# Kernel optimization log

Measured on AMD Instinct MI355X. Metric: run time of the kernel, lower is better.

The kernel has to match this reference:

```python
import jax, jax.numpy as jnp
import numpy as np

B, S, D, H, KH, DH, L, V, MULT = 1, 2048, 2048, 16, 2, 128, 4, 10000, 4
INNER = D * MULT
EPS = 1e-5


def layernorm(x, g, b):
    m = jnp.mean(x, axis=-1, keepdims=True)
    v = jnp.var(x, axis=-1, keepdims=True)
    return (x - m) * jax.lax.rsqrt(v + EPS) * g + b


def setup_inputs() -> dict:
    key = jax.random.key(0)
    ks = jax.random.split(key, 24)
    s = lambda *shape: 0.02
    inp = {
        'text': jax.random.randint(ks[0], (B, S), 0, V),
        'embed_w': jax.random.normal(ks[1], (V, D), jnp.float32) * 0.02,
        # model-level LayerNorm (applied after embed and after every block)
        'model_norm_g': jnp.ones((D,), jnp.float32),
        'model_norm_b': jnp.zeros((D,), jnp.float32),
        # per-block params, stacked on leading L axis
        'blk_norm_g': jnp.ones((L, D), jnp.float32),
        'blk_norm_b': jnp.zeros((L, D), jnp.float32),
        'attn_norm_g': jnp.ones((L, D), jnp.float32),  # RingAttention prenorm
        'attn_norm_b': jnp.zeros((L, D), jnp.float32),
        'wq': jax.random.normal(ks[2], (L, D, H * DH), jnp.float32) * 0.02,
        'wk': jax.random.normal(ks[3], (L, D, KH * DH), jnp.float32) * 0.02,
        'wv': jax.random.normal(ks[4], (L, D, KH * DH), jnp.float32) * 0.02,
        'wo': jax.random.normal(ks[5], (L, H * DH, D), jnp.float32) * 0.02,
        'qn_g': jnp.ones((L, DH), jnp.float32),  # qk_norm LayerNorm scales
        'kn_g': jnp.ones((L, DH), jnp.float32),
        'w1': jax.random.normal(ks[6], (L, D, INNER), jnp.float32) * 0.02,
        'b1': jnp.zeros((L, INNER), jnp.float32),
        'w2': jax.random.normal(ks[7], (L, INNER, D), jnp.float32) * 0.02,
        'b2': jnp.zeros((L, D), jnp.float32),
        # output head: LayerNorm + Linear(D, V)
        'head_norm_g': jnp.ones((D,), jnp.float32),
        'head_norm_b': jnp.zeros((D,), jnp.float32),
        'head_w': jax.random.normal(ks[8], (D, V), jnp.float32) * 0.02,
        'head_b': jnp.zeros((V,), jnp.float32),
    }
    return inp


def _attention(xn, wq, wk, wv, wo, qn_g, kn_g):
    # xn: [B,S,D] (already prenormed)
    q = (xn @ wq).reshape(B, S, H, DH)
    k = (xn @ wk).reshape(B, S, KH, DH)
    v = (xn @ wv).reshape(B, S, KH, DH)
    # qk-norm: LayerNorm over head dim with learnable scale
    q = layernorm(q, qn_g, 0.0)
    k = layernorm(k, kn_g, 0.0)
    # GQA: expand kv heads to query heads
    rep = H // KH
    k = jnp.repeat(k, rep, axis=2)  # [B,S,H,DH]
    v = jnp.repeat(v, rep, axis=2)
    scale = DH ** -0.5
    scores = jnp.einsum('bqhd,bkhd->bhqk', q, k) * scale  # [B,H,S,S]
    causal = jnp.tril(jnp.ones((S, S), bool))
    scores = jnp.where(causal, scores, jnp.finfo(scores.dtype).min)
    p = jax.nn.softmax(scores, axis=-1)
    out = jnp.einsum('bhqk,bkhd->bqhd', p, v).reshape(B, S, H * DH)
    return out @ wo


def reference(text, embed_w, model_norm_g, model_norm_b, blk_norm_g, blk_norm_b,
              attn_norm_g, attn_norm_b, wq, wk, wv, wo, qn_g, kn_g,
              w1, b1, w2, b2, head_norm_g, head_norm_b, head_w, head_b):
    x = embed_w[text]                                # [B,S,D]
    x = layernorm(x, model_norm_g, model_norm_b)
    for i in range(L):
        h = layernorm(x, blk_norm_g[i], blk_norm_b[i])       # block norm
        hn = layernorm(h, attn_norm_g[i], attn_norm_b[i])    # attn prenorm
        h = _attention(hn, wq[i], wk[i], wv[i], wo[i], qn_g[i], kn_g[i]) + h
        ff = jax.nn.gelu(h @ w1[i] + b1[i]) @ w2[i] + b2[i]
        x = ff + h
        x = layernorm(x, model_norm_g, model_norm_b)
    x = layernorm(x, head_norm_g, head_norm_b)
    return x @ head_w + head_b                       # [B,S,V] logits
```

## Files before the change

kernel.cpp:

```cpp
#include <hip/hip_runtime.h>
#include <math.h>

#define S_LEN 2048
#define DMODEL 2048
#define NHEAD 16
#define KVHEAD 2
#define DHEAD 128
#define NLAYER 4
#define VOCAB 10000
#define INNER_DIM 8192
#define LN_EPS 1e-5f
#define VOCAB_PAD 10240
#define QKVN 2560

typedef __attribute__((ext_vector_type(4))) float f32x4;
typedef __attribute__((ext_vector_type(2))) float f32x2;
typedef __attribute__((ext_vector_type(8))) short s16x8;
typedef __attribute__((ext_vector_type(4))) short s16x4;

__device__ __forceinline__ short f2bf(float f) {
  union { float f; unsigned u; } v; v.f = f;
  unsigned r = v.u + 0x7FFFu + ((v.u >> 16) & 1u);
  return (short)(r >> 16);
}

__device__ __forceinline__ float gelu_tanh(float x) {
  float z = 0.7978845608028654f * (x + 0.044715f * x * x * x);
  float t = __expf(-2.0f * fabsf(z));
  float th = (1.0f - t) / (1.0f + t);
  th = copysignf(th, z);
  return 0.5f * x * (1.0f + th);
}

__device__ __forceinline__ void glds16(const void* g, void* l) {
  __builtin_amdgcn_global_load_lds(
      (const __attribute__((address_space(1))) unsigned int*)g,
      (__attribute__((address_space(3))) unsigned int*)l, 16, 0, 0);
}

__global__ __launch_bounds__(256)
void wtrans_all(const float* __restrict__ wq, const float* __restrict__ wk,
                const float* __restrict__ wv, const float* __restrict__ wo,
                const float* __restrict__ w1, const float* __restrict__ w2,
                short* __restrict__ wqkvT, short* __restrict__ woT,
                short* __restrict__ w1T, short* __restrict__ w2T) {
  __shared__ float ld[64][65];
  int b = blockIdx.x;
  const float* W; short* WT; int gx, K;
  if (b < 1024)      { W = wq; WT = wqkvT; gx = 32; K = 2048; }
  else if (b < 1152) { b -= 1024; W = wk; WT = wqkvT + (size_t)2048 * 2048; gx = 4; K = 2048; }
  else if (b < 1280) { b -= 1152; W = wv; WT = wqkvT + (size_t)2304 * 2048; gx = 4; K = 2048; }
  else if (b < 2304) { b -= 1280; W = wo; WT = woT; gx = 32; K = 2048; }
  else if (b < 6400) { b -= 2304; W = w1; WT = w1T; gx = 128; K = 2048; }
  else               { b -= 6400; W = w2; WT = w2T; gx = 32; K = 8192; }
  const int N = gx * 64;
  const int n0 = (b % gx) * 64, k0 = (b / gx) * 64;
  const int tid = threadIdx.x;
  const int rbase = tid >> 4;
  const int c4 = (tid & 15) * 4;
#pragma unroll
  for (int q = 0; q < 4; ++q) {
    int kk = rbase + q * 16;
    f32x4 v = *(const f32x4*)(W + (size_t)(k0 + kk) * N + n0 + c4);
    ld[kk][c4 + 0] = v[0]; ld[kk][c4 + 1] = v[1];
    ld[kk][c4 + 2] = v[2]; ld[kk][c4 + 3] = v[3];
  }
  __syncthreads();
#pragma unroll
  for (int s = 0; s < 2; ++s) {
    int lin = tid + s * 256;
    int nn = lin >> 3;
    int ks = lin & 7;
    s16x8 o;
#pragma unroll
    for (int j = 0; j < 8; ++j) o[j] = f2bf(ld[ks * 8 + j][nn]);
    *(s16x8*)&WT[(size_t)(n0 + nn) * K + k0 + ks * 8] = o;
  }
}

__global__ __launch_bounds__(256)
void wtrans64(const float* __restrict__ W, short* __restrict__ WT,
              int K, int N, int NP) {
  __shared__ float ld[64][65];
  const int n0 = blockIdx.x * 64, k0 = blockIdx.y * 64;
  const int tid = threadIdx.x;
  const int rbase = tid >> 4;
  const int c4 = (tid & 15) * 4;
#pragma unroll
  for (int q = 0; q < 4; ++q) {
    int kk = rbase + q * 16;
    const float* wp = W + (size_t)(k0 + kk) * N + n0 + c4;
    float v0, v1, v2, v3;
    if (n0 + c4 + 3 < N) {
      f32x4 v = *(const f32x4*)wp;
      v0 = v[0]; v1 = v[1]; v2 = v[2]; v3 = v[3];
    } else {
      v0 = (n0 + c4 + 0 < N) ? wp[0] : 0.f;
      v1 = (n0 + c4 + 1 < N) ? wp[1] : 0.f;
      v2 = (n0 + c4 + 2 < N) ? wp[2] : 0.f;
      v3 = (n0 + c4 + 3 < N) ? wp[3] : 0.f;
    }
    ld[kk][c4 + 0] = v0; ld[kk][c4 + 1] = v1;
    ld[kk][c4 + 2] = v2; ld[kk][c4 + 3] = v3;
  }
  __syncthreads();
#pragma unroll
  for (int s = 0; s < 2; ++s) {
    int lin = tid + s * 256;
    int nn = lin >> 3;
    int ks = lin & 7;
    int n = n0 + nn;
    if (n < NP) {
      s16x8 o;
#pragma unroll
      for (int j = 0; j < 8; ++j)
        o[j] = (n < N) ? f2bf(ld[ks * 8 + j][nn]) : (short)0;
      *(s16x8*)&WT[(size_t)n * K + k0 + ks * 8] = o;
    }
  }
}

__device__ __forceinline__ void ln3_core(
    float (&v)[8], int tid, int wave,
    const float* __restrict__ mg, const float* __restrict__ mb,
    const float* __restrict__ bg, const float* __restrict__ bb,
    const float* __restrict__ ag, const float* __restrict__ ab,
    float* __restrict__ hbrow, short* __restrict__ hnrow,
    float rs[3][4], float rs2[3][4]) {
#pragma unroll
  for (int rnd = 0; rnd < 3; ++rnd) {
    float s = 0.f, s2 = 0.f;
#pragma unroll
    for (int i = 0; i < 8; ++i) { s += v[i]; s2 += v[i] * v[i]; }
#pragma unroll
    for (int off = 1; off < 64; off <<= 1) {
      s += __shfl_xor(s, off); s2 += __shfl_xor(s2, off);
    }
    if ((tid & 63) == 0) { rs[rnd][wave] = s; rs2[rnd][wave] = s2; }
    __syncthreads();
    s = rs[rnd][0] + rs[rnd][1] + rs[rnd][2] + rs[rnd][3];
    s2 = rs2[rnd][0] + rs2[rnd][1] + rs2[rnd][2] + rs2[rnd][3];
    const float mean = s * (1.f / DMODEL);
    const float var = s2 * (1.f / DMODEL) - mean * mean;
    const float rstd = rsqrtf(var + LN_EPS);
    const float* gg = (rnd == 0) ? mg : (rnd == 1) ? bg : ag;
    const float* bbv = (rnd == 0) ? mb : (rnd == 1) ? bb : ab;
#pragma unroll
    for (int i = 0; i < 8; ++i) {
      int idx = tid + i * 256;
      v[i] = (v[i] - mean) * rstd * gg[idx] + bbv[idx];
    }
    if (rnd == 1) {
#pragma unroll
      for (int i = 0; i < 8; ++i) hbrow[tid + i * 256] = v[i];
    }
  }
#pragma unroll
  for (int i = 0; i < 8; ++i) hnrow[tid + i * 256] = f2bf(v[i]);
}

__global__ __launch_bounds__(256)
void ln_triple(const float* __restrict__ in,
               const float* __restrict__ mg, const float* __restrict__ mb,
               const float* __restrict__ bg, const float* __restrict__ bb,
               const float* __restrict__ ag, const float* __restrict__ ab,
               float* __restrict__ hb, short* __restrict__ hn16) {
  const int row = blockIdx.x;
  const int tid = threadIdx.x;
  const int wave = tid >> 6;
  __shared__ float rs[3][4], rs2[3][4];
  float v[8];
  const float* x = in + (size_t)row * DMODEL;
#pragma unroll
  for (int i = 0; i < 8; ++i) v[i] = x[tid + i * 256];
  ln3_core(v, tid, wave, mg, mb, bg, bb, ag, ab,
           hb + (size_t)row * DMODEL, hn16 + (size_t)row * DMODEL, rs, rs2);
}

__global__ __launch_bounds__(256)
void embed_ln3(const int* __restrict__ text, const float* __restrict__ ew,
               const float* __restrict__ mg, const float* __restrict__ mb,
               const float* __restrict__ bg, const float* __restrict__ bb,
               const float* __restrict__ ag, const float* __restrict__ ab,
               float* __restrict__ hb, short* __restrict__ hn16) {
  const int row = blockIdx.x;
  const int tid = threadIdx.x;
  const int wave = tid >> 6;
  __shared__ float rs[3][4], rs2[3][4];
  float v[8];
  const float* x = ew + (size_t)text[row] * DMODEL;
#pragma unroll
  for (int i = 0; i < 8; ++i) v[i] = x[tid + i * 256];
  ln3_core(v, tid, wave, mg, mb, bg, bb, ag, ab,
           hb + (size_t)row * DMODEL, hn16 + (size_t)row * DMODEL, rs, rs2);
}

__global__ __launch_bounds__(256)
void ln_dual(const float* __restrict__ in,
             const float* __restrict__ mg, const float* __restrict__ mb,
             const float* __restrict__ hg, const float* __restrict__ hbv,
             short* __restrict__ out16) {
  const int row = blockIdx.x;
  const int tid = threadIdx.x;
  const int wave = tid >> 6;
  __shared__ float rs[2][4], rs2[2][4];
  float v[8];
  const float* x = in + (size_t)row * DMODEL;
#pragma unroll
  for (int i = 0; i < 8; ++i) v[i] = x[tid + i * 256];
#pragma unroll
  for (int rnd = 0; rnd < 2; ++rnd) {
    float s = 0.f, s2 = 0.f;
#pragma unroll
    for (int i = 0; i < 8; ++i) { s += v[i]; s2 += v[i] * v[i]; }
#pragma unroll
    for (int off = 1; off < 64; off <<= 1) {
      s += __shfl_xor(s, off); s2 += __shfl_xor(s2, off);
    }
    if ((tid & 63) == 0) { rs[rnd][wave] = s; rs2[rnd][wave] = s2; }
    __syncthreads();
    s = rs[rnd][0] + rs[rnd][1] + rs[rnd][2] + rs[rnd][3];
    s2 = rs2[rnd][0] + rs2[rnd][1] + rs2[rnd][2] + rs2[rnd][3];
    const float mean = s * (1.f / DMODEL);
    const float var = s2 * (1.f / DMODEL) - mean * mean;
    const float rstd = rsqrtf(var + LN_EPS);
    const float* gg = (rnd == 0) ? mg : hg;
    const float* bbv = (rnd == 0) ? mb : hbv;
#pragma unroll
    for (int i = 0; i < 8; ++i) {
      int idx = tid + i * 256;
      v[i] = (v[i] - mean) * rstd * gg[idx] + bbv[idx];
    }
  }
  short* o = out16 + (size_t)row * DMODEL;
#pragma unroll
  for (int i = 0; i < 8; ++i) o[tid + i * 256] = f2bf(v[i]);
}

template<int BM, int BN, int BK, int WM, int WN, int ACT, bool BIAS, bool RES,
         bool WF, bool WB>
__global__ __launch_bounds__(WM * WN * 64)
void gemm_db(const short* __restrict__ A, const short* __restrict__ BT,
             const float* __restrict__ bias, const float* __restrict__ res,
             float* __restrict__ Cf, short* __restrict__ Cb,
             int M, int N, int K) {
  constexpr int THREADS = WM * WN * 64;
  constexpr int MR = BM / WM / 16;
  constexpr int NR = BN / WN / 16;
  constexpr int KH = BK / 32;
  constexpr int SLOTS = BK / 8;
  constexpr int SMASK = SLOTS - 1;
  constexpr int RSH = (SLOTS == 8) ? 0 : 1;
  constexpr int CSH = (SLOTS == 8) ? 3 : 2;
  constexpr int NI = (BM * BK) / (THREADS * 8);
  __shared__ short As[2][BM * BK];
  __shared__ short Bs[2][BN * BK];
  const int tid = threadIdx.x;
  const int wave = tid >> 6, lane = tid & 63;
  const int g = lane >> 4, r = lane & 15;
  const int wm = wave / WN, wn = wave % WN;

  const int GY = gridDim.y;
  int lin = blockIdx.x + blockIdx.y * gridDim.x;
  int nwg = gridDim.x * GY;
  int sw = ((nwg & 7) == 0) ? ((lin & 7) * (nwg >> 3) + (lin >> 3)) : lin;
  const int bm = (sw % GY) * BM;
  const int bn = (sw / GY) * BN;

  const short* gsrc[2 * NI];
  short* ldst[2][2 * NI];
#pragma unroll
  for (int i = 0; i < NI; ++i) {
    int c = i * THREADS + tid;
    int row = c >> CSH;
    int slot = c & SMASK;
    int col = ((slot ^ ((row >> RSH) & SMASK)) << 3);
    gsrc[i] = A + (size_t)(bm + row) * K + col;
    gsrc[NI + i] = BT + (size_t)(bn + row) * K + col;
    int base = (i * THREADS + (wave << 6)) << 3;
    ldst[0][i] = &As[0][base]; ldst[0][NI + i] = &Bs[0][base];
    ldst[1][i] = &As[1][base]; ldst[1][NI + i] = &Bs[1][base];
  }

  f32x4 acc[MR][NR] = {};
  const int NT = K / BK;

#pragma unroll
  for (int i = 0; i < 2 * NI; ++i) glds16(gsrc[i], ldst[0][i]);
  asm volatile("s_waitcnt vmcnt(0)" ::: "memory");
  __syncthreads();

  for (int t = 0; t < NT; ++t) {
    const int cur = t & 1;
    const short* as = As[cur];
    const short* bs = Bs[cur];
    s16x8 bfr[NR][KH], af[MR / 2][KH];
#pragma unroll
    for (int n = 0; n < NR; ++n) {
      int rr = wn * (NR * 16) + n * 16 + r;
#pragma unroll
      for (int kk = 0; kk < KH; ++kk) {
        int lg = kk * 4 + g;
        bfr[n][kk] = *(const s16x8*)&bs[rr * BK + ((lg ^ ((rr >> RSH) & SMASK)) << 3)];
      }
    }
#pragma unroll
    for (int mm = 0; mm < MR / 2; ++mm) {
      int rr = wm * (MR * 16) + mm * 16 + r;
#pragma unroll
      for (int kk = 0; kk < KH; ++kk) {
        int lg = kk * 4 + g;
        af[mm][kk] = *(const s16x8*)&as[rr * BK + ((lg ^ ((rr >> RSH) & SMASK)) << 3)];
      }
    }
    if (t + 1 < NT) {
#pragma unroll
      for (int i = 0; i < 2 * NI; ++i) glds16(gsrc[i] + (t + 1) * BK, ldst[cur ^ 1][i]);
    }
    asm volatile("s_waitcnt lgkmcnt(0)" ::: "memory");
    __builtin_amdgcn_sched_barrier(0);
    __builtin_amdgcn_s_setprio(1);
#pragma unroll
    for (int mm = 0; mm < MR / 2; ++mm)
#pragma unroll
      for (int n = 0; n < NR; ++n)
#pragma unroll
        for (int kk = 0; kk < KH; ++kk)
          acc[mm][n] = __builtin_amdgcn_mfma_f32_16x16x32_bf16(af[mm][kk], bfr[n][kk], acc[mm][n], 0, 0, 0);
    __builtin_amdgcn_s_setprio(0);
    __builtin_amdgcn_s_barrier();
#pragma unroll
    for (int mm = 0; mm < MR / 2; ++mm) {
      int rr = wm * (MR * 16) + (MR / 2 + mm) * 16 + r;
#pragma unroll
      for (int kk = 0; kk < KH; ++kk) {
        int lg = kk * 4 + g;
        af[mm][kk] = *(const s16x8*)&as[rr * BK + ((lg ^ ((rr >> RSH) & SMASK)) << 3)];
      }
    }
    asm volatile("s_waitcnt lgkmcnt(0)" ::: "memory");
    __builtin_amdgcn_sched_barrier(0);
    __builtin_amdgcn_s_setprio(1);
#pragma unroll
    for (int mm = 0; mm < MR / 2; ++mm)
#pragma unroll
      for (int n = 0; n < NR; ++n)
#pragma unroll
        for (int kk = 0; kk < KH; ++kk)
          acc[MR / 2 + mm][n] = __builtin_amdgcn_mfma_f32_16x16x32_bf16(af[mm][kk], bfr[n][kk], acc[MR / 2 + mm][n], 0, 0, 0);
    __builtin_amdgcn_s_setprio(0);
    __syncthreads();
  }

#pragma unroll
  for (int m = 0; m < MR; ++m) {
    int row = bm + wm * (MR * 16) + m * 16 + g * 4;
#pragma unroll
    for (int n = 0; n < NR; ++n) {
      int col = bn + wn * (NR * 16) + n * 16 + r;
      if (col < N) {
#pragma unroll
        for (int j = 0; j < 4; ++j) {
          float v = acc[m][n][j];
          if (BIAS) v += bias[col];
          if (ACT) v = gelu_tanh(v);
          if (RES) v += res[(size_t)(row + j) * N + col];
          if (WF) Cf[(size_t)(row + j) * N + col] = v;
          if (WB) Cb[(size_t)(row + j) * N + col] = f2bf(v);
        }
      }
    }
  }
}

__global__ __launch_bounds__(256)
void gemm_qkv(const short* __restrict__ A, const short* __restrict__ BT,
              const float* __restrict__ qg, const float* __restrict__ kg,
              short* __restrict__ qb, short* __restrict__ kb,
              short* __restrict__ vt, int M, int K) {
  __shared__ short As[2][128 * 64];
  __shared__ short Bs[2][128 * 64];
  __shared__ float rsm[2][128], rs2m[2][128];
  const int tid = threadIdx.x;
  const int wave = tid >> 6, lane = tid & 63;
  const int g = lane >> 4, r = lane & 15;
  const int wm = wave >> 1, wn = wave & 1;

  const int GY = gridDim.y;
  int lin = blockIdx.x + blockIdx.y * gridDim.x;
  int nwg = gridDim.x * GY;
  int sw = (lin & 7) * (nwg >> 3) + (lin >> 3);
  const int bm = (sw % GY) * 128;
  const int bn = (sw / GY) * 128;

  const short* gsrc[8];
  short* ldst[2][8];
#pragma unroll
  for (int i = 0; i < 4; ++i) {
    int c = i * 256 + tid;
    int row = c >> 3;
    int slot = c & 7;
    int col = ((slot ^ (row & 7)) << 3);
    gsrc[i] = A + (size_t)(bm + row) * K + col;
    gsrc[4 + i] = BT + (size_t)(bn + row) * K + col;
    int base = (i * 256 + (wave << 6)) << 3;
    ldst[0][i] = &As[0][base]; ldst[0][4 + i] = &Bs[0][base];
    ldst[1][i] = &As[1][base]; ldst[1][4 + i] = &Bs[1][base];
  }

  f32x4 acc[4][4] = {};
  const int NT = K >> 6;

#pragma unroll
  for (int i = 0; i < 8; ++i) glds16(gsrc[i], ldst[0][i]);
  asm volatile("s_waitcnt vmcnt(0)" ::: "memory");
  __syncthreads();

  for (int t = 0; t < NT; ++t) {
    const int cur = t & 1;
    const short* as = As[cur];
    const short* bs = Bs[cur];
    s16x8 bfr[4][2], af[2][2];
#pragma unroll
    for (int n = 0; n < 4; ++n) {
      int rr = wn * 64 + n * 16 + r;
#pragma unroll
      for (int kk = 0; kk < 2; ++kk) {
        int lg = kk * 4 + g;
        bfr[n][kk] = *(const s16x8*)&bs[rr * 64 + ((lg ^ (rr & 7)) << 3)];
      }
    }
#pragma unroll
    for (int mm = 0; mm < 2; ++mm) {
      int rr = wm * 64 + mm * 16 + r;
#pragma unroll
      for (int kk = 0; kk < 2; ++kk) {
        int lg = kk * 4 + g;
        af[mm][kk] = *(const s16x8*)&as[rr * 64 + ((lg ^ (rr & 7)) << 3)];
      }
    }
    if (t + 1 < NT) {
#pragma unroll
      for (int i = 0; i < 8; ++i) glds16(gsrc[i] + (t + 1) * 64, ldst[cur ^ 1][i]);
    }
    asm volatile("s_waitcnt lgkmcnt(0)" ::: "memory");
    __builtin_amdgcn_sched_barrier(0);
    __builtin_amdgcn_s_setprio(1);
#pragma unroll
    for (int mm = 0; mm < 2; ++mm)
#pragma unroll
      for (int n = 0; n < 4; ++n)
#pragma unroll
        for (int kk = 0; kk < 2; ++kk)
          acc[mm][n] = __builtin_amdgcn_mfma_f32_16x16x32_bf16(af[mm][kk], bfr[n][kk], acc[mm][n], 0, 0, 0);
    __builtin_amdgcn_s_setprio(0);
    __builtin_amdgcn_s_barrier();
#pragma unroll
    for (int mm = 0; mm < 2; ++mm) {
      int rr = wm * 64 + (2 + mm) * 16 + r;
#pragma unroll
      for (int kk = 0; kk < 2; ++kk) {
        int lg = kk * 4 + g;
        af[mm][kk] = *(const s16x8*)&as[rr * 64 + ((lg ^ (rr & 7)) << 3)];
      }
    }
    asm volatile("s_waitcnt lgkmcnt(0)" ::: "memory");
    __builtin_amdgcn_sched_barrier(0);
    __builtin_amdgcn_s_setprio(1);
#pragma unroll
    for (int mm = 0; mm < 2; ++mm)
#pragma unroll
      for (int n = 0; n < 4; ++n)
#pragma unroll
        for (int kk = 0; kk < 2; ++kk)
          acc[2 + mm][n] = __builtin_amdgcn_mfma_f32_16x16x32_bf16(af[mm][kk], bfr[n][kk], acc[2 + mm][n], 0, 0, 0);
    __builtin_amdgcn_s_setprio(0);
    __syncthreads();
  }

  if (bn >= 2304) {
    short* ld = &As[0][0];
#pragma unroll
    for (int m = 0; m < 4; ++m) {
      int sl = wm * 64 + m * 16 + g * 4;
#pragma unroll
      for (int n = 0; n < 4; ++n) {
        int dl = wn * 64 + n * 16 + r;
#pragma unroll
        for (int j = 0; j < 4; ++j)
          ld[(sl + j) * 128 + dl] = f2bf(acc[m][n][j]);
      }
    }
    __syncthreads();
    const int dl = tid & 127;
    const int sh = (tid >> 7) * 64;
    short* dst = vt + (size_t)(bn - 2304 + dl) * S_LEN + bm + sh;
#pragma unroll
    for (int v = 0; v < 8; ++v) {
      s16x8 o;
#pragma unroll
      for (int i = 0; i < 8; ++i) o[i] = ld[(sh + v * 8 + i) * 128 + dl];
      *(s16x8*)(dst + v * 8) = o;
    }
  } else {
    float ms[4][4], m2[4][4];
#pragma unroll
    for (int m = 0; m < 4; ++m)
#pragma unroll
      for (int j = 0; j < 4; ++j) {
        float s = 0.f, s2 = 0.f;
#pragma unroll
        for (int n = 0; n < 4; ++n) { float v = acc[m][n][j]; s += v; s2 += v * v; }
#pragma unroll
        for (int off = 1; off < 16; off <<= 1) {
          s += __shfl_xor(s, off); s2 += __shfl_xor(s2, off);
        }
        ms[m][j] = s; m2[m][j] = s2;
      }
    if (r == 0) {
#pragma unroll
      for (int m = 0; m < 4; ++m)
#pragma unroll
        for (int j = 0; j < 4; ++j) {
          int rl = wm * 64 + m * 16 + g * 4 + j;
          rsm[wn][rl] = ms[m][j]; rs2m[wn][rl] = m2[m][j];
        }
    }
    __syncthreads();
    const float* gv = (bn < 2048) ? qg : kg;
#pragma unroll
    for (int m = 0; m < 4; ++m)
#pragma unroll
      for (int j = 0; j < 4; ++j) {
        int rl = wm * 64 + m * 16 + g * 4 + j;
        float s = rsm[0][rl] + rsm[1][rl];
        float s2 = rs2m[0][rl] + rs2m[1][rl];
        float mean = s * (1.f / 128.f);
        float var = s2 * (1.f / 128.f) - mean * mean;
        float rstd = rsqrtf(var + LN_EPS);
        int srow = bm + rl;
#pragma unroll
        for (int n = 0; n < 4; ++n) {
          int cl = wn * 64 + n * 16 + r;
          float v = (acc[m][n][j] - mean) * rstd * gv[cl];
          if (bn < 2048) qb[(size_t)srow * 2048 + bn + cl] = f2bf(v);
          else kb[(size_t)srow * 256 + (bn - 2048) + cl] = f2bf(v);
        }
      }
  }
}

__global__ __launch_bounds__(256)
void attn_fwd3(const short* __restrict__ qbuf, const short* __restrict__ kbuf,
               const short* __restrict__ vtb, short* __restrict__ obuf) {
  __shared__ short Qs[64 * 128];
  __shared__ short Ks[64 * 128];
  __shared__ short Vt[128 * 64];
  __shared__ short Ps[4][16][88];
  const int tid = threadIdx.x;
  int lin = blockIdx.x + blockIdx.y * gridDim.x;
  int sw = (lin & 7) * 32 + (lin >> 3);
  const int pair = sw & 15;
  const int h = sw >> 4;
  const int kh = h >> 3;
  const int wave = tid >> 6, lane = tid & 63;
  const int g = lane >> 4, r = lane & 15;
  const float scale = 0.08838834764831845f;

#pragma unroll
  for (int half = 0; half < 2; ++half) {
    const int qt = half ? (31 - pair) : pair;
    const int qbase = qt * 64;
    __builtin_amdgcn_s_barrier();
#pragma unroll
    for (int i = 0; i < 4; ++i) {
      int c = i * 256 + tid;
      int row = c >> 4;
      int scol = (((c & 15) ^ (row & 7)) << 3);
      glds16(qbuf + (size_t)(qbase + row) * DMODEL + h * DHEAD + scol,
             &Qs[(i * 256 + (wave << 6)) << 3]);
    }
    f32x4 O[8] = {};
    float mst[4], lst[4];
#pragma unroll
    for (int j = 0; j < 4; ++j) { mst[j] = -1e30f; lst[j] = 0.f; }
    s16x8 aq[4];

    for (int jt = 0; jt <= qt; ++jt) {
      const int jb = jt * 64;
      if (jt) __builtin_amdgcn_s_barrier();
#pragma unroll
      for (int i = 0; i < 4; ++i) {
        int c = i * 256 + tid;
        int row = c >> 4;
        int scol = (((c & 15) ^ (row & 7)) << 3);
        glds16(kbuf + (size_t)(jb + row) * 256 + kh * DHEAD + scol,
               &Ks[(i * 256 + (wave << 6)) << 3]);
      }
#pragma unroll
      for (int i = 0; i < 4; ++i) {
        int c = i * 256 + tid;
        int row = c >> 3;
        int scol = (((c & 7) ^ (row & 7)) << 3);
        glds16(vtb + (size_t)(kh * 128 + row) * S_LEN + jb + scol,
               &Vt[(i * 256 + (wave << 6)) << 3]);
      }
      asm volatile("s_waitcnt vmcnt(4)" ::: "memory");
      __builtin_amdgcn_s_barrier();
      if (jt == 0) {
#pragma unroll
        for (int kc = 0; kc < 4; ++kc) {
          int rr = wave * 16 + r;
          aq[kc] = *(const s16x8*)&Qs[rr * 128 + ((((kc << 2) | g) ^ (rr & 7)) << 3)];
        }
      }
      f32x4 sc[4] = {};
      __builtin_amdgcn_s_setprio(1);
#pragma unroll
      for (int n = 0; n < 4; ++n) {
        int rr = n * 16 + r;
#pragma unroll
        for (int kc = 0; kc < 4; ++kc) {
          s16x8 bk = *(const s16x8*)&Ks[rr * 128 + ((((kc << 2) | g) ^ (rr & 7)) << 3)];
          sc[n] = __builtin_amdgcn_mfma_f32_16x16x32_bf16(aq[kc], bk, sc[n], 0, 0, 0);
        }
      }
      __builtin_amdgcn_s_setprio(0);
      if (jt == qt) {
#pragma unroll
        for (int j = 0; j < 4; ++j) {
          int irow = qbase + wave * 16 + g * 4 + j;
#pragma unroll
          for (int n = 0; n < 4; ++n) {
            int jcol = jb + n * 16 + r;
            sc[n][j] = (jcol <= irow) ? sc[n][j] * scale : -1e30f;
          }
        }
      } else {
#pragma unroll
        for (int j = 0; j < 4; ++j)
#pragma unroll
          for (int n = 0; n < 4; ++n) sc[n][j] *= scale;
      }
      float pmax[4], alpha[4], rsum[4];
#pragma unroll
      for (int j = 0; j < 4; ++j)
        pmax[j] = fmaxf(fmaxf(sc[0][j], sc[1][j]), fmaxf(sc[2][j], sc[3][j]));
#pragma unroll
      for (int off = 1; off < 16; off <<= 1)
#pragma unroll
        for (int j = 0; j < 4; ++j) pmax[j] = fmaxf(pmax[j], __shfl_xor(pmax[j], off));
#pragma unroll
      for (int j = 0; j < 4; ++j) {
        float mnew = fmaxf(mst[j], pmax[j]);
        alpha[j] = __expf(mst[j] - mnew);
        mst[j] = mnew;
#pragma unroll
        for (int n = 0; n < 4; ++n) sc[n][j] = __expf(sc[n][j] - mnew);
        rsum[j] = (sc[0][j] + sc[1][j]) + (sc[2][j] + sc[3][j]);
      }
#pragma unroll
      for (int off = 1; off < 16; off <<= 1)
#pragma unroll
        for (int j = 0; j < 4; ++j) rsum[j] += __shfl_xor(rsum[j], off);
#pragma unroll
      for (int j = 0; j < 4; ++j) lst[j] = lst[j] * alpha[j] + rsum[j];
#pragma unroll
      for (int d = 0; d < 8; ++d)
#pragma unroll
        for (int j = 0; j < 4; ++j) O[d][j] *= alpha[j];
      asm volatile("s_waitcnt vmcnt(0)" ::: "memory");
      __builtin_amdgcn_s_barrier();
#pragma unroll
      for (int j = 0; j < 4; ++j)
#pragma unroll
        for (int n = 0; n < 4; ++n)
          Ps[wave][g * 4 + j][n * 16 + r] = f2bf(sc[n][j]);
      s16x8 pa0 = *(const s16x8*)&Ps[wave][r][g * 8];
      s16x8 pa1 = *(const s16x8*)&Ps[wave][r][32 + g * 8];
      __builtin_amdgcn_s_setprio(1);
#pragma unroll
      for (int d = 0; d < 8; ++d) {
        int dd = d * 16 + r;
        s16x8 b0 = *(const s16x8*)&Vt[dd * 64 + ((g ^ (dd & 7)) << 3)];
        s16x8 b1 = *(const s16x8*)&Vt[dd * 64 + (((4 + g) ^ (dd & 7)) << 3)];
        O[d] = __builtin_amdgcn_mfma_f32_16x16x32_bf16(pa0, b0, O[d], 0, 0, 0);
        O[d] = __builtin_amdgcn_mfma_f32_16x16x32_bf16(pa1, b1, O[d], 0, 0, 0);
      }
      __builtin_amdgcn_s_setprio(0);
    }
    float linv[4];
#pragma unroll
    for (int j = 0; j < 4; ++j) linv[j] = 1.f / lst[j];
#pragma unroll
    for (int d = 0; d < 8; ++d)
#pragma unroll
      for (int j = 0; j < 4; ++j)
        obuf[(size_t)(qbase + wave * 16 + g * 4 + j) * DMODEL + h * DHEAD + d * 16 + r] =
            f2bf(O[d][j] * linv[j]);
  }
}

extern "C" void kernel_launch(void* const* d_in, const int* in_sizes, int n_in,
                              void* d_out, int out_size, void* d_ws, size_t ws_size,
                              hipStream_t stream) {
  const int* text = (const int*)d_in[0];
  const float* embed_w = (const float*)d_in[1];
  const float* model_g = (const float*)d_in[2];
  const float* model_b = (const float*)d_in[3];
  const float* blk_g = (const float*)d_in[4];
  const float* blk_b = (const float*)d_in[5];
  const float* attn_g = (const float*)d_in[6];
  const float* attn_b = (const float*)d_in[7];
  const float* wq = (const float*)d_in[8];
  const float* wk = (const float*)d_in[9];
  const float* wv = (const float*)d_in[10];
  const float* wo = (const float*)d_in[11];
  const float* qn_g = (const float*)d_in[12];
  const float* kn_g = (const float*)d_in[13];
  const float* w1 = (const float*)d_in[14];
  const float* b1 = (const float*)d_in[15];
  const float* w2 = (const float*)d_in[16];
  const float* b2 = (const float*)d_in[17];
  const float* head_g = (const float*)d_in[18];
  const float* head_b = (const float*)d_in[19];
  const float* head_w = (const float*)d_in[20];
  const float* head_bias = (const float*)d_in[21];
  float* out = (float*)d_out;

  const size_t SD = (size_t)S_LEN * DMODEL;
  const size_t SKV = (size_t)S_LEN * KVHEAD * DHEAD;
  const size_t SI = (size_t)S_LEN * INNER_DIM;
  const size_t WD = (size_t)DMODEL * DMODEL;
  const size_t WKV = (size_t)DMODEL * KVHEAD * DHEAD;
  const size_t WI = (size_t)DMODEL * INNER_DIM;

  char* p = (char*)d_ws;
  float* xres  = (float*)p; p += SD * 4;
  float* hb    = (float*)p; p += SD * 4;
  float* h2    = (float*)p; p += SD * 4;
  short* hn16  = (short*)p; p += SD * 2;
  short* h216  = (short*)p; p += SD * 2;
  short* ao16  = (short*)p; p += SD * 2;
  short* ffi16 = (short*)p; p += SI * 2;
  short* qb16  = (short*)p; p += SD * 2;
  short* kb16  = (short*)p; p += SKV * 2;
  short* vt16  = (short*)p; p += SKV * 2;
  short* wqkvT = (short*)p; p += (size_t)QKVN * DMODEL * 2;
  short* woT   = (short*)p; p += WD * 2;
  short* w1T   = (short*)p; p += WI * 2;
  short* w2T   = (short*)p; p += WI * 2;
  short* headT = w1T;

  dim3 blk(256);
  embed_ln3<<<S_LEN, blk, 0, stream>>>(text, embed_w, model_g, model_b,
                                       blk_g, blk_b, attn_g, attn_b, hb, hn16);

  for (int i = 0; i < NLAYER; ++i) {
    wtrans_all<<<10496, blk, 0, stream>>>(
        wq + (size_t)i * WD, wk + (size_t)i * WKV, wv + (size_t)i * WKV,
        wo + (size_t)i * WD, w1 + (size_t)i * WI, w2 + (size_t)i * WI,
        wqkvT, woT, w1T, w2T);

    gemm_qkv<<<dim3(QKVN / 128, S_LEN / 128), blk, 0, stream>>>(
        hn16, wqkvT, qn_g + i * DHEAD, kn_g + i * DHEAD,
        qb16, kb16, vt16, S_LEN, DMODEL);

    attn_fwd3<<<dim3(16, 16), blk, 0, stream>>>(qb16, kb16, vt16, ao16);

    gemm_db<128, 128, 64, 2, 2, 0, false, true, true, true>
        <<<dim3(DMODEL / 128, S_LEN / 128), blk, 0, stream>>>(
        ao16, woT, nullptr, hb, h2, h216, S_LEN, DMODEL, DMODEL);
    gemm_db<256, 256, 64, 2, 4, 1, true, false, false, true>
        <<<dim3(INNER_DIM / 256, S_LEN / 256), dim3(512), 0, stream>>>(
        h216, w1T, b1 + (size_t)i * INNER_DIM, nullptr, nullptr, ffi16,
        S_LEN, INNER_DIM, DMODEL);
    gemm_db<128, 128, 64, 2, 2, 0, true, true, true, false>
        <<<dim3(DMODEL / 128, S_LEN / 128), blk, 0, stream>>>(
        ffi16, w2T, b2 + (size_t)i * DMODEL, h2, xres, nullptr, S_LEN, DMODEL, INNER_DIM);

    if (i + 1 < NLAYER) {
      ln_triple<<<S_LEN, blk, 0, stream>>>(
          xres, model_g, model_b,
          blk_g + (i + 1) * DMODEL, blk_b + (i + 1) * DMODEL,
          attn_g + (i + 1) * DMODEL, attn_b + (i + 1) * DMODEL, hb, hn16);
    }
  }

  wtrans64<<<dim3(VOCAB_PAD / 64, 32), blk, 0, stream>>>(head_w, headT, DMODEL, VOCAB, VOCAB_PAD);
  ln_dual<<<S_LEN, blk, 0, stream>>>(xres, model_g, model_b, head_g, head_b, hn16);
  gemm_db<256, 256, 64, 2, 4, 0, true, false, true, false>
      <<<dim3(VOCAB_PAD / 256, S_LEN / 256), dim3(512), 0, stream>>>(
      hn16, headT, head_bias, nullptr, out, nullptr, S_LEN, VOCAB, DMODEL);
}
```

Before: 1.641 ms.

## Split-K the FFN down-projection and fold the partial-sum reduction into the layernorm

The W2 GEMM (K=8192) now runs as a two-way split-K into two fp32 partial buffers, giving twice as many workgroups over the 16x16 tile grid. The residual, bias and partial sums are then added inside new ln_triple_sum and ln_dual_sum kernels, so the fp32 h2 and xres buffers go away. The residual is now read back from the bf16 h216 copy, which loses precision. The FFN-up and head GEMMs also move from 256x256 to 128x128 tiles, raising workgroup count at the cost of more operand traffic.

```diff
diff --git a/kernel.cpp b/kernel.cpp
--- a/kernel.cpp
+++ b/kernel.cpp
@@ -22,6 +22,10 @@
   union { float f; unsigned u; } v; v.f = f;
   unsigned r = v.u + 0x7FFFu + ((v.u >> 16) & 1u);
   return (short)(r >> 16);
+}
+__device__ __forceinline__ float bf2f(short s) {
+  union { unsigned u; float f; } v; v.u = ((unsigned)(unsigned short)s) << 16;
+  return v.f;
 }
 
 __device__ __forceinline__ float gelu_tanh(float x) {
@@ -160,24 +164,6 @@
 }
 
 __global__ __launch_bounds__(256)
-void ln_triple(const float* __restrict__ in,
-               const float* __restrict__ mg, const float* __restrict__ mb,
-               const float* __restrict__ bg, const float* __restrict__ bb,
-               const float* __restrict__ ag, const float* __restrict__ ab,
-               float* __restrict__ hb, short* __restrict__ hn16) {
-  const int row = blockIdx.x;
-  const int tid = threadIdx.x;
-  const int wave = tid >> 6;
-  __shared__ float rs[3][4], rs2[3][4];
-  float v[8];
-  const float* x = in + (size_t)row * DMODEL;
-#pragma unroll
-  for (int i = 0; i < 8; ++i) v[i] = x[tid + i * 256];
-  ln3_core(v, tid, wave, mg, mb, bg, bb, ag, ab,
-           hb + (size_t)row * DMODEL, hn16 + (size_t)row * DMODEL, rs, rs2);
-}
-
-__global__ __launch_bounds__(256)
 void embed_ln3(const int* __restrict__ text, const float* __restrict__ ew,
                const float* __restrict__ mg, const float* __restrict__ mb,
                const float* __restrict__ bg, const float* __restrict__ bb,
@@ -196,18 +182,44 @@
 }
 
 __global__ __launch_bounds__(256)
-void ln_dual(const float* __restrict__ in,
-             const float* __restrict__ mg, const float* __restrict__ mb,
-             const float* __restrict__ hg, const float* __restrict__ hbv,
-             short* __restrict__ out16) {
+void ln_triple_sum(const float* __restrict__ p0, const float* __restrict__ p1,
+                   const short* __restrict__ h216, const float* __restrict__ b2,
+                   const float* __restrict__ mg, const float* __restrict__ mb,
+                   const float* __restrict__ bg, const float* __restrict__ bb,
+                   const float* __restrict__ ag, const float* __restrict__ ab,
+                   float* __restrict__ hb, short* __restrict__ hn16) {
+  const int row = blockIdx.x;
+  const int tid = threadIdx.x;
+  const int wave = tid >> 6;
+  __shared__ float rs[3][4], rs2[3][4];
+  float v[8];
+  const size_t base = (size_t)row * DMODEL;
+#pragma unroll
+  for (int i = 0; i < 8; ++i) {
+    int idx = tid + i * 256;
+    v[i] = p0[base + idx] + p1[base + idx] + b2[idx] + bf2f(h216[base + idx]);
+  }
+  ln3_core(v, tid, wave, mg, mb, bg, bb, ag, ab,
+           hb + base, hn16 + base, rs, rs2);
+}
+
+__global__ __launch_bounds__(256)
+void ln_dual_sum(const float* __restrict__ p0, const float* __restrict__ p1,
+                 const short* __restrict__ h216, const float* __restrict__ b2,
+                 const float* __restrict__ mg, const float* __restrict__ mb,
+                 const float* __restrict__ hg, const float* __restrict__ hbv,
+                 short* __restrict__ out16) {
   const int row = blockIdx.x;
   const int tid = threadIdx.x;
   const int wave = tid >> 6;
   __shared__ float rs[2][4], rs2[2][4];
   float v[8];
-  const float* x = in + (size_t)row * DMODEL;
-#pragma unroll
-  for (int i = 0; i < 8; ++i) v[i] = x[tid + i * 256];
+  const size_t base = (size_t)row * DMODEL;
+#pragma unroll
+  for (int i = 0; i < 8; ++i) {
+    int idx = tid + i * 256;
+    v[i] = p0[base + idx] + p1[base + idx] + b2[idx] + bf2f(h216[base + idx]);
+  }
 #pragma unroll
   for (int rnd = 0; rnd < 2; ++rnd) {
     float s = 0.f, s2 = 0.f;
@@ -232,18 +244,18 @@
       v[i] = (v[i] - mean) * rstd * gg[idx] + bbv[idx];
     }
   }
-  short* o = out16 + (size_t)row * DMODEL;
+  short* o = out16 + base;
 #pragma unroll
   for (int i = 0; i < 8; ++i) o[tid + i * 256] = f2bf(v[i]);
 }
 
 template<int BM, int BN, int BK, int WM, int WN, int ACT, bool BIAS, bool RES,
-         bool WF, bool WB>
+         bool WF, bool WB, bool SPLITK>
 __global__ __launch_bounds__(WM * WN * 64)
 void gemm_db(const short* __restrict__ A, const short* __restrict__ BT,
              const float* __restrict__ bias, const float* __restrict__ res,
              float* __restrict__ Cf, short* __restrict__ Cb,
-             int M, int N, int K) {
+             int M, int N, int K, int LDA, int LDB) {
   constexpr int THREADS = WM * WN * 64;
   constexpr int MR = BM / WM / 16;
   constexpr int NR = BN / WN / 16;
@@ -259,6 +271,8 @@
   const int wave = tid >> 6, lane = tid & 63;
   const int g = lane >> 4, r = lane & 15;
   const int wm = wave / WN, wn = wave % WN;
+  const int zoff = SPLITK ? blockIdx.z * K : 0;
+  if (SPLITK && WF) Cf += (size_t)blockIdx.z * M * N;
 
   const int GY = gridDim.y;
   int lin = blockIdx.x + blockIdx.y * gridDim.x;
@@ -275,8 +289,8 @@
     int row = c >> CSH;
     int slot = c & SMASK;
     int col = ((slot ^ ((row >> RSH) & SMASK)) << 3);
-    gsrc[i] = A + (size_t)(bm + row) * K + col;
-    gsrc[NI + i] = BT + (size_t)(bn + row) * K + col;
+    gsrc[i] = A + (size_t)(bm + row) * LDA + zoff + col;
+    gsrc[NI + i] = BT + (size_t)(bn + row) * LDB + zoff + col;
     int base = (i * THREADS + (wave << 6)) << 3;
     ldst[0][i] = &As[0][base]; ldst[0][NI + i] = &Bs[0][base];
     ldst[1][i] = &As[1][base]; ldst[1][NI + i] = &Bs[1][base];
@@ -736,9 +750,8 @@
   const size_t WI = (size_t)DMODEL * INNER_DIM;
 
   char* p = (char*)d_ws;
-  float* xres  = (float*)p; p += SD * 4;
   float* hb    = (float*)p; p += SD * 4;
-  float* h2    = (float*)p; p += SD * 4;
+  float* wpart = (float*)p; p += SD * 4 * 2;
   short* hn16  = (short*)p; p += SD * 2;
   short* h216  = (short*)p; p += SD * 2;
   short* ao16  = (short*)p; p += SD * 2;
@@ -768,28 +781,35 @@
 
     attn_fwd3<<<dim3(16, 16), blk, 0, stream>>>(qb16, kb16, vt16, ao16);
 
-    gemm_db<128, 128, 64, 2, 2, 0, false, true, true, true>
+    gemm_db<128, 128, 64, 2, 2, 0, false, true, false, true, false>
         <<<dim3(DMODEL / 128, S_LEN / 128), blk, 0, stream>>>(
-        ao16, woT, nullptr, hb, h2, h216, S_LEN, DMODEL, DMODEL);
-    gemm_db<256, 256, 64, 2, 4, 1, true, false, false, true>
-        <<<dim3(INNER_DIM / 256, S_LEN / 256), dim3(512), 0, stream>>>(
+        ao16, woT, nullptr, hb, nullptr, h216,
+        S_LEN, DMODEL, DMODEL, DMODEL, DMODEL);
+    gemm_db<128, 128, 64, 2, 2, 1, true, false, false, true, false>
+        <<<dim3(INNER_DIM / 128, S_LEN / 128), blk, 0, stream>>>(
         h216, w1T, b1 + (size_t)i * INNER_DIM, nullptr, nullptr, ffi16,
-        S_LEN, INNER_DIM, DMODEL);
-    gemm_db<128, 128, 64, 2, 2, 0, true, true, true, false>
-        <<<dim3(DMODEL / 128, S_LEN / 128), blk, 0, stream>>>(
-        ffi16, w2T, b2 + (size_t)i * DMODEL, h2, xres, nullptr, S_LEN, DMODEL, INNER_DIM);
+        S_LEN, INNER_DIM, DMODEL, DMODEL, DMODEL);
+    gemm_db<128, 128, 64, 2, 2, 0, false, false, true, false, true>
+        <<<dim3(DMODEL / 128, S_LEN / 128, 2), blk, 0, stream>>>(
+        ffi16, w2T, nullptr, nullptr, wpart, nullptr,
+        S_LEN, DMODEL, INNER_DIM / 2, INNER_DIM, INNER_DIM);
 
     if (i + 1 < NLAYER) {
-      ln_triple<<<S_LEN, blk, 0, stream>>>(
-          xres, model_g, model_b,
+      ln_triple_sum<<<S_LEN, blk, 0, stream>>>(
+          wpart, wpart + SD, h216, b2 + (size_t)i * DMODEL,
+          model_g, model_b,
           blk_g + (i + 1) * DMODEL, blk_b + (i + 1) * DMODEL,
           attn_g + (i + 1) * DMODEL, attn_b + (i + 1) * DMODEL, hb, hn16);
+    } else {
+      ln_dual_sum<<<S_LEN, blk, 0, stream>>>(
+          wpart, wpart + SD, h216, b2 + (size_t)i * DMODEL,
+          model_g, model_b, head_g, head_b, hn16);
     }
   }
 
   wtrans64<<<dim3(VOCAB_PAD / 64, 32), blk, 0, stream>>>(head_w, headT, DMODEL, VOCAB, VOCAB_PAD);
-  ln_dual<<<S_LEN, blk, 0, stream>>>(xres, model_g, model_b, head_g, head_b, hn16);
-  gemm_db<256, 256, 64, 2, 4, 0, true, false, true, false>
-      <<<dim3(VOCAB_PAD / 256, S_LEN / 256), dim3(512), 0, stream>>>(
-      hn16, headT, head_bias, nullptr, out, nullptr, S_LEN, VOCAB, DMODEL);
-}
+  gemm_db<128, 128, 64, 2, 2, 0, true, false, true, false, false>
+      <<<dim3(VOCAB_PAD / 128, S_LEN / 128), blk, 0, stream>>>(
+      hn16, headT, head_bias, nullptr, out, nullptr,
+      S_LEN, VOCAB, DMODEL, DMODEL, DMODEL);
+}
```

After: 1.514 ms. -7.7%, faster.
